# Kernel tuning notes

Hardware: AMD Instinct MI355X
Metric: run time of the kernel (lower is better)

Reference implementation:

```python
import jax, jax.numpy as jnp
import numpy as np

H = 64  # hidden_size

def _xavier(key, shape):
    fan_in, fan_out = shape[1], shape[0]
    limit = float(np.sqrt(6.0 / (fan_in + fan_out)))
    return jax.random.uniform(key, shape, jnp.float32, -limit, limit)

def setup_inputs() -> dict:
    key = jax.random.key(0)
    ks = jax.random.split(key, 4)
    B, T, I = 4096, 512, 1
    x = jax.random.normal(ks[0], (B, T, I), jnp.float32)
    W_ih = _xavier(ks[1], (H, I))      # input->hidden
    W_hh = _xavier(ks[2], (H, H))      # hidden->hidden
    b_ih = jnp.zeros((H,), jnp.float32)
    b_hh = jnp.zeros((H,), jnp.float32)
    fc_w = _xavier(ks[3], (1, H))      # final linear
    fc_b = jnp.zeros((1,), jnp.float32)
    return {"x": x, "W_ih": W_ih, "W_hh": W_hh, "b_ih": b_ih,
            "b_hh": b_hh, "fc_w": fc_w, "fc_b": fc_b}

def reference(x, W_ih, W_hh, b_ih, b_hh, fc_w, fc_b):
    # Precompute input projection for all timesteps: [B, T, H]
    xw = jnp.einsum('bti,hi->bth', x, W_ih) + b_ih
    h0 = jnp.zeros((x.shape[0], H), x.dtype)

    def step(h, xw_t):
        h = jnp.tanh(xw_t + h @ W_hh.T + b_hh)
        return h, None

    # scan over time (axis 0 after transpose): sequential recurrence
    h_last, _ = jax.lax.scan(step, h0, jnp.swapaxes(xw, 0, 1))
    return h_last @ fc_w.T + fc_b  # [B, 1]
```

## Files before the change

kernel.cpp:

```cpp
#include <hip/hip_runtime.h>
#include <stdint.h>

#define HDIM 64
#define TDIM 512
#define GB   16


typedef float    f32x4 __attribute__((ext_vector_type(4)));
typedef _Float16 f16x8 __attribute__((ext_vector_type(8)));
typedef _Float16 f16x2 __attribute__((ext_vector_type(2)));
typedef unsigned int u32;
typedef unsigned int u32x2 __attribute__((ext_vector_type(2)));
typedef unsigned int u32x4 __attribute__((ext_vector_type(4)));

__device__ __forceinline__ u32 pk2(float a, float b) {
    return __builtin_bit_cast(u32, __builtin_amdgcn_cvt_pkrtz(a, b));
}
__device__ __forceinline__ float hi_mask(float v) {
    return __builtin_bit_cast(float, __builtin_bit_cast(u32, v) & 0xFFFFE000u);
}

__global__ __launch_bounds__(256, 1)
__attribute__((amdgpu_waves_per_eu(1)))
void rnn_pingpong(const float* __restrict__ x,
                  const float* __restrict__ W_ih,
                  const float* __restrict__ W_hh,
                  const float* __restrict__ b_ih,
                  const float* __restrict__ b_hh,
                  const float* __restrict__ fc_w,
                  const float* __restrict__ fc_b,
                  float* __restrict__ out,
                  int B)
{
    __shared__ __align__(16) u32 st[2][4][64][4];
    __shared__ float xs[64][GB];
    __shared__ float red[4][GB];

    const int tid  = threadIdx.x;
    const int lane = tid & 63;
    const int w    = tid >> 6;
    const int b    = lane & 15;
    const int g    = lane >> 4;
    const int m16  = lane & 15;
    const int gb0  = blockIdx.x * GB;
    const int wc   = w >> 1;
    const int wh   = w & 1;

    const float K = 2.885390081777927f;

    f16x8 Ahi0, Ahi1, Alo0, Alo1;
    {
        const int wr = 32*wc + 8*(m16 >> 2) + 4*wh + (m16 & 3);
        const float* wrow = W_hh + wr * HDIM;
        const f32x4 va0 = *(const f32x4*)(wrow + 8*g);
        const f32x4 vb0 = *(const f32x4*)(wrow + 8*g + 4);
        const f32x4 va1 = *(const f32x4*)(wrow + 32 + 8*g);
        const f32x4 vb1 = *(const f32x4*)(wrow + 32 + 8*g + 4);
#pragma unroll
        for (int e = 0; e < 4; ++e) {
            float v; _Float16 h;
            v = K*va0[e]; h = (_Float16)v; Ahi0[e]   = h; Alo0[e]   = (_Float16)(v - (float)h);
            v = K*vb0[e]; h = (_Float16)v; Ahi0[e+4] = h; Alo0[e+4] = (_Float16)(v - (float)h);
            v = K*va1[e]; h = (_Float16)v; Ahi1[e]   = h; Alo1[e]   = (_Float16)(v - (float)h);
            v = K*vb1[e]; h = (_Float16)v; Ahi1[e+4] = h; Alo1[e+4] = (_Float16)(v - (float)h);
        }
    }

    float wihc[4], biasc[4];
#pragma unroll
    for (int r = 0; r < 4; ++r) {
        const int idx = 32*wc + 8*g + 4*wh + r;
        wihc[r]  = K * W_ih[idx];
        biasc[r] = K * (b_ih[idx] + b_hh[idx]);
    }

    {
        const u32x4 z = {0u, 0u, 0u, 0u};
        ((u32x4*)st)[tid]       = z;
        ((u32x4*)st)[tid + 256] = z;
    }

    const int sm = tid >> 4;
    const int tq = tid & 15;
    const f32x4 zero4 = {0.f, 0.f, 0.f, 0.f};

    float hv0 = 0.f, hv1 = 0.f, hv2 = 0.f, hv3 = 0.f;

#pragma unroll 1
    for (int tc = 0; tc < TDIM/64; ++tc) {
        const f32x4 xv4 = *(const f32x4*)(x + (size_t)(gb0 + sm) * TDIM
                                            + tc*64 + tq*4);
        xs[tq*4 + 0][sm] = xv4.x;
        xs[tq*4 + 1][sm] = xv4.y;
        xs[tq*4 + 2][sm] = xv4.z;
        xs[tq*4 + 3][sm] = xv4.w;
        __syncthreads();

#pragma unroll 1
        for (int tj = 0; tj < 64; ++tj) {
            const int pp = tj & 1;
            const f16x8 ih0 = __builtin_bit_cast(f16x8, *(const u32x4*)&st[pp][0][lane][0]);
            const f16x8 ih1 = __builtin_bit_cast(f16x8, *(const u32x4*)&st[pp][1][lane][0]);
            const f16x8 il0 = __builtin_bit_cast(f16x8, *(const u32x4*)&st[pp][2][lane][0]);
            const f16x8 il1 = __builtin_bit_cast(f16x8, *(const u32x4*)&st[pp][3][lane][0]);
            const float xt = xs[tj][b];

            f32x4 c1, c1b, c2, c2b, c3, c3b;
            c1.x = fmaf(xt, wihc[0], biasc[0]);
            c1.y = fmaf(xt, wihc[1], biasc[1]);
            c1.z = fmaf(xt, wihc[2], biasc[2]);
            c1.w = fmaf(xt, wihc[3], biasc[3]);
            c1b = zero4; c2 = zero4; c2b = zero4; c3 = zero4; c3b = zero4;

            c1  = __builtin_amdgcn_mfma_f32_16x16x32_f16(Ahi0, ih0, c1,  0, 0, 0);
            c1b = __builtin_amdgcn_mfma_f32_16x16x32_f16(Ahi1, ih1, c1b, 0, 0, 0);
            c2  = __builtin_amdgcn_mfma_f32_16x16x32_f16(Ahi0, il0, c2,  0, 0, 0);
            c2b = __builtin_amdgcn_mfma_f32_16x16x32_f16(Ahi1, il1, c2b, 0, 0, 0);
            c3  = __builtin_amdgcn_mfma_f32_16x16x32_f16(Alo0, ih0, c3,  0, 0, 0);
            c3b = __builtin_amdgcn_mfma_f32_16x16x32_f16(Alo1, ih1, c3b, 0, 0, 0);

            const f32x4 zsum = (c1 + c1b) + ((c2 + c2b) + (c3 + c3b));

            hv0 = fmaf(-2.0f, __builtin_amdgcn_rcpf(__builtin_amdgcn_exp2f(zsum.x) + 1.0f), 1.0f);
            hv1 = fmaf(-2.0f, __builtin_amdgcn_rcpf(__builtin_amdgcn_exp2f(zsum.y) + 1.0f), 1.0f);
            hv2 = fmaf(-2.0f, __builtin_amdgcn_rcpf(__builtin_amdgcn_exp2f(zsum.z) + 1.0f), 1.0f);
            hv3 = fmaf(-2.0f, __builtin_amdgcn_rcpf(__builtin_amdgcn_exp2f(zsum.w) + 1.0f), 1.0f);

            const float h0 = hi_mask(hv0), h1 = hi_mask(hv1);
            const float h2 = hi_mask(hv2), h3 = hi_mask(hv3);
            u32x2 nh, nl;
            nh.x = pk2(h0, h1);           nh.y = pk2(h2, h3);
            nl.x = pk2(hv0-h0, hv1-h1);   nl.y = pk2(hv2-h2, hv3-h3);

            *(u32x2*)&st[pp ^ 1][wc][lane][2*wh]     = nh;
            *(u32x2*)&st[pp ^ 1][2 + wc][lane][2*wh] = nl;
            __syncthreads();
        }
    }

    float acc = 0.0f;
    acc = fmaf(hv0, fc_w[32*wc + 8*g + 4*wh + 0], acc);
    acc = fmaf(hv1, fc_w[32*wc + 8*g + 4*wh + 1], acc);
    acc = fmaf(hv2, fc_w[32*wc + 8*g + 4*wh + 2], acc);
    acc = fmaf(hv3, fc_w[32*wc + 8*g + 4*wh + 3], acc);
    acc += __shfl_xor(acc, 16, 64);
    acc += __shfl_xor(acc, 32, 64);
    if (lane < 16) red[w][lane] = acc;
    __syncthreads();
    if (tid < GB)
        out[gb0 + tid] = red[0][tid] + red[1][tid] + red[2][tid] + red[3][tid]
                       + fc_b[0];
}

extern "C" void kernel_launch(void* const* d_in, const int* in_sizes, int n_in,
                              void* d_out, int out_size, void* d_ws, size_t ws_size,
                              hipStream_t stream)
{
    const float* x    = (const float*)d_in[0];
    const float* W_ih = (const float*)d_in[1];
    const float* W_hh = (const float*)d_in[2];
    const float* b_ih = (const float*)d_in[3];
    const float* b_hh = (const float*)d_in[4];
    const float* fc_w = (const float*)d_in[5];
    const float* fc_b = (const float*)d_in[6];
    float* out = (float*)d_out;

    const int B = in_sizes[0] / TDIM;
    const int blocks = B / GB;

    rnn_pingpong<<<blocks, 256, 0, stream>>>(
        x, W_ih, W_hh, b_ih, b_hh, fc_w, fc_b, out, B);
}
```

Baseline: 226.5 us.

## Pack two independent batch teams into each 512-thread block

Doubles the block to 512 threads so each block runs two independent 16-sequence recurrences (teams), each with its own ping-pong state and x staging buffers in shared memory. The intent is to interleave the two teams' latency-bound MFMA and transcendental chains on one CU to hide per-step latency. In exchange the grid shrinks to half as many blocks, so only half the CUs may be occupied. The per-step __syncthreads now also couples both teams, so either team's stalls hold up the other.

```diff
diff --git a/kernel.cpp b/kernel.cpp
--- a/kernel.cpp
+++ b/kernel.cpp
@@ -4,11 +4,11 @@
 #define HDIM 64
 #define TDIM 512
 #define GB   16
+#define NT   2
 
 
 typedef float    f32x4 __attribute__((ext_vector_type(4)));
 typedef _Float16 f16x8 __attribute__((ext_vector_type(8)));
-typedef _Float16 f16x2 __attribute__((ext_vector_type(2)));
 typedef unsigned int u32;
 typedef unsigned int u32x2 __attribute__((ext_vector_type(2)));
 typedef unsigned int u32x4 __attribute__((ext_vector_type(4)));
@@ -20,9 +20,8 @@
     return __builtin_bit_cast(float, __builtin_bit_cast(u32, v) & 0xFFFFE000u);
 }
 
-__global__ __launch_bounds__(256, 1)
-__attribute__((amdgpu_waves_per_eu(1)))
-void rnn_pingpong(const float* __restrict__ x,
+__global__ __launch_bounds__(512, 2)
+void rnn_dualteam(const float* __restrict__ x,
                   const float* __restrict__ W_ih,
                   const float* __restrict__ W_hh,
                   const float* __restrict__ b_ih,
@@ -32,17 +31,19 @@
                   float* __restrict__ out,
                   int B)
 {
-    __shared__ __align__(16) u32 st[2][4][64][4];
-    __shared__ float xs[64][GB];
-    __shared__ float red[4][GB];
+    __shared__ __align__(16) u32 st[NT][2][4][64][4];
+    __shared__ float xs[NT][64][GB];
+    __shared__ float red[NT][4][GB];
 
     const int tid  = threadIdx.x;
+    const int ttid = tid & 255;
+    const int team = tid >> 8;
     const int lane = tid & 63;
-    const int w    = tid >> 6;
+    const int w    = (tid >> 6) & 3;
     const int b    = lane & 15;
     const int g    = lane >> 4;
     const int m16  = lane & 15;
-    const int gb0  = blockIdx.x * GB;
+    const int gb0  = blockIdx.x * (GB * NT) + team * GB;
     const int wc   = w >> 1;
     const int wh   = w & 1;
 
@@ -77,11 +78,11 @@
     {
         const u32x4 z = {0u, 0u, 0u, 0u};
         ((u32x4*)st)[tid]       = z;
-        ((u32x4*)st)[tid + 256] = z;
+        ((u32x4*)st)[tid + 512] = z;
     }
 
-    const int sm = tid >> 4;
-    const int tq = tid & 15;
+    const int sm = ttid >> 4;
+    const int tq = ttid & 15;
     const f32x4 zero4 = {0.f, 0.f, 0.f, 0.f};
 
     float hv0 = 0.f, hv1 = 0.f, hv2 = 0.f, hv3 = 0.f;
@@ -90,20 +91,20 @@
     for (int tc = 0; tc < TDIM/64; ++tc) {
         const f32x4 xv4 = *(const f32x4*)(x + (size_t)(gb0 + sm) * TDIM
                                             + tc*64 + tq*4);
-        xs[tq*4 + 0][sm] = xv4.x;
-        xs[tq*4 + 1][sm] = xv4.y;
-        xs[tq*4 + 2][sm] = xv4.z;
-        xs[tq*4 + 3][sm] = xv4.w;
+        xs[team][tq*4 + 0][sm] = xv4.x;
+        xs[team][tq*4 + 1][sm] = xv4.y;
+        xs[team][tq*4 + 2][sm] = xv4.z;
+        xs[team][tq*4 + 3][sm] = xv4.w;
         __syncthreads();
 
 #pragma unroll 1
         for (int tj = 0; tj < 64; ++tj) {
             const int pp = tj & 1;
-            const f16x8 ih0 = __builtin_bit_cast(f16x8, *(const u32x4*)&st[pp][0][lane][0]);
-            const f16x8 ih1 = __builtin_bit_cast(f16x8, *(const u32x4*)&st[pp][1][lane][0]);
-            const f16x8 il0 = __builtin_bit_cast(f16x8, *(const u32x4*)&st[pp][2][lane][0]);
-            const f16x8 il1 = __builtin_bit_cast(f16x8, *(const u32x4*)&st[pp][3][lane][0]);
-            const float xt = xs[tj][b];
+            const f16x8 ih0 = __builtin_bit_cast(f16x8, *(const u32x4*)&st[team][pp][0][lane][0]);
+            const f16x8 ih1 = __builtin_bit_cast(f16x8, *(const u32x4*)&st[team][pp][1][lane][0]);
+            const f16x8 il0 = __builtin_bit_cast(f16x8, *(const u32x4*)&st[team][pp][2][lane][0]);
+            const f16x8 il1 = __builtin_bit_cast(f16x8, *(const u32x4*)&st[team][pp][3][lane][0]);
+            const float xt = xs[team][tj][b];
 
             f32x4 c1, c1b, c2, c2b, c3, c3b;
             c1.x = fmaf(xt, wihc[0], biasc[0]);
@@ -132,8 +133,8 @@
             nh.x = pk2(h0, h1);           nh.y = pk2(h2, h3);
             nl.x = pk2(hv0-h0, hv1-h1);   nl.y = pk2(hv2-h2, hv3-h3);
 
-            *(u32x2*)&st[pp ^ 1][wc][lane][2*wh]     = nh;
-            *(u32x2*)&st[pp ^ 1][2 + wc][lane][2*wh] = nl;
+            *(u32x2*)&st[team][pp ^ 1][wc][lane][2*wh]     = nh;
+            *(u32x2*)&st[team][pp ^ 1][2 + wc][lane][2*wh] = nl;
             __syncthreads();
         }
     }
@@ -145,11 +146,11 @@
     acc = fmaf(hv3, fc_w[32*wc + 8*g + 4*wh + 3], acc);
     acc += __shfl_xor(acc, 16, 64);
     acc += __shfl_xor(acc, 32, 64);
-    if (lane < 16) red[w][lane] = acc;
+    if (lane < 16) red[team][w][lane] = acc;
     __syncthreads();
-    if (tid < GB)
-        out[gb0 + tid] = red[0][tid] + red[1][tid] + red[2][tid] + red[3][tid]
-                       + fc_b[0];
+    if (ttid < GB)
+        out[gb0 + ttid] = red[team][0][ttid] + red[team][1][ttid]
+                        + red[team][2][ttid] + red[team][3][ttid] + fc_b[0];
 }
 
 extern "C" void kernel_launch(void* const* d_in, const int* in_sizes, int n_in,
@@ -166,8 +167,8 @@
     float* out = (float*)d_out;
 
     const int B = in_sizes[0] / TDIM;
-    const int blocks = B / GB;
+    const int blocks = B / (GB * NT);
 
-    rnn_pingpong<<<blocks, 256, 0, stream>>>(
+    rnn_dualteam<<<blocks, 512, 0, stream>>>(
         x, W_ih, W_hh, b_ih, b_hh, fc_w, fc_b, out, B);
 }
```

Measured after the change: 267.1 us. +17.9%, slower.
